# Kernel optimization log

Measured on AMD Instinct MI355X. Metric: run time of the kernel, lower is better.

Reference implementation:

```python
import jax, jax.numpy as jnp
import numpy as np

B, S, D, H = 2, 2048, 1024, 16
DK = D // H
NEG = -1e9


def setup_inputs() -> dict:
    key = jax.random.key(0)
    ks = jax.random.split(key, 12)
    inp = {
        "query": jax.random.normal(ks[0], (B, S, D), jnp.float32),
        "key": jax.random.normal(ks[1], (B, S, D), jnp.float32),
        "value": jax.random.normal(ks[2], (B, S, D), jnp.float32),
        "mask": jax.random.randint(ks[3], (B, S), 0, 2, jnp.int32),
    }
    # 4 linears (q, k, v, out), each d_model x d_model with bias.
    scale = 1.0 / np.sqrt(D)
    for i, name in enumerate(["wq", "wk", "wv", "wo"]):
        inp[name] = jax.random.uniform(ks[4 + i], (D, D), jnp.float32, -scale, scale)
        inp["b" + name[1]] = jax.random.uniform(ks[8 + i], (D,), jnp.float32, -scale, scale)
    return inp


def _split_heads(x):  # [B,S,D] -> [B,H,S,DK]
    return x.reshape(B, S, H, DK).transpose(0, 2, 1, 3)


def reference(query, key, value, mask, wq, bq, wk, bk, wv, bv, wo, bo):
    q = _split_heads(query @ wq.T + bq)
    k = _split_heads(key @ wk.T + bk)
    v = _split_heads(value @ wv.T + bv)
    scores = jnp.einsum("bhqd,bhkd->bhqk", q, k) / jnp.sqrt(jnp.float32(DK))
    # mask: [B,S] -> [B,1,1,S]; masked_fill where mask == 0
    m = mask[:, None, None, :]
    scores = jnp.where(m == 0, NEG, scores)
    attn = jax.nn.softmax(scores, axis=-1)  # dropout p=0 (eval) -> identity
    x = jnp.einsum("bhqk,bhkd->bhqd", attn, v)
    x = x.transpose(0, 2, 1, 3).reshape(B, S, D)
    return x @ wo.T + bo
```

## Files before the change

kernel.cpp:

```cpp
#include <hip/hip_runtime.h>


typedef _Float16 f16;
typedef _Float16 f16x8 __attribute__((ext_vector_type(8)));
typedef _Float16 f16x4 __attribute__((ext_vector_type(4)));
typedef __fp16 fp16x2r __attribute__((ext_vector_type(2)));
typedef float f32x4 __attribute__((ext_vector_type(4)));

#define MFMA_F16(a, b, c) __builtin_amdgcn_mfma_f32_16x16x32_f16((a), (b), (c), 0, 0, 0)
#define L2E 1.44269504088896340736f

__device__ __forceinline__ void gld16(const void* g, void* l) {
    __builtin_amdgcn_global_load_lds(
        (__attribute__((address_space(1))) void*)(g),
        (__attribute__((address_space(3))) void*)(l), 16, 0, 0);
}

__global__ __launch_bounds__(256) void cvt_kernel(
    const float* __restrict__ q, const float* __restrict__ k,
    const float* __restrict__ v,
    const float* __restrict__ wq, const float* __restrict__ wk,
    const float* __restrict__ wv, const float* __restrict__ wo,
    f16* __restrict__ oq, f16* __restrict__ ok, f16* __restrict__ ov,
    f16* __restrict__ owq, f16* __restrict__ owk, f16* __restrict__ owv,
    f16* __restrict__ owo)
{
    const int z = blockIdx.y;
    const float* src;
    f16* dst;
    int n;
    switch (z) {
        case 0: src = q;  dst = oq;  n = 4194304; break;
        case 1: src = k;  dst = ok;  n = 4194304; break;
        case 2: src = v;  dst = ov;  n = 4194304; break;
        case 3: src = wq; dst = owq; n = 1048576; break;
        case 4: src = wk; dst = owk; n = 1048576; break;
        case 5: src = wv; dst = owv; n = 1048576; break;
        default: src = wo; dst = owo; n = 1048576; break;
    }
    int idx = (blockIdx.x * 256 + threadIdx.x) * 8;
    if (idx >= n) return;
    float4 a = *(const float4*)(src + idx);
    float4 b = *(const float4*)(src + idx + 4);
    f16x8 h = { (f16)a.x, (f16)a.y, (f16)a.z, (f16)a.w,
                (f16)b.x, (f16)b.y, (f16)b.z, (f16)b.w };
    *(f16x8*)(dst + idx) = h;
}

__device__ __forceinline__ void stage_qkv(
    const f16* __restrict__ P0, const f16* __restrict__ P1,
    int blockM, int blockN, int k0, f16* Ad, f16* Bd,
    int wave, int srow2, int schunk)
{
#pragma unroll
    for (int p = 0; p < 2; p++) {
        int r0 = wave * 32 + p * 16;
        gld16(&P0[(size_t)(blockM + r0 + srow2) * 1024 + k0 + schunk * 8],
              &Ad[r0 * 32]);
        gld16(&P1[(size_t)(blockN + r0 + srow2) * 1024 + k0 + schunk * 8],
              &Bd[r0 * 32]);
    }
}

__global__ __launch_bounds__(256) void proj_qkv_kernel(
    const f16* __restrict__ xq, const f16* __restrict__ xk,
    const f16* __restrict__ xv,
    const f16* __restrict__ wqh, const f16* __restrict__ wkh,
    const f16* __restrict__ wvh,
    const float* __restrict__ bq, const float* __restrict__ bk,
    const float* __restrict__ bv,
    f16* __restrict__ qh, f16* __restrict__ kh, f16* __restrict__ vt)
{
    const int z = blockIdx.z;
    const f16* X = (z == 0) ? xq : (z == 1) ? xk : xv;
    const f16* W = (z == 0) ? wqh : (z == 1) ? wkh : wvh;
    const float* bias = (z == 0) ? bq : (z == 1) ? bk : bv;
    const f16* P0 = (z < 2) ? W : X;
    const f16* P1 = (z < 2) ? X : W;

    __shared__ __align__(16) f16 smem[24576];
    f16* L = smem;

    const int t = threadIdx.x;
    const int wave = t >> 6, lane = t & 63, quad = lane >> 4, l15 = lane & 15;
    const int m_base = (wave >> 1) * 64, n_base = (wave & 1) * 64;
    const int blockM = (z < 2) ? blockIdx.y * 128 : blockIdx.x * 128;
    const int blockN = (z < 2) ? blockIdx.x * 128 : blockIdx.y * 128;

    const int srow2 = lane >> 2;
    const int schunk = (lane & 3) ^ ((srow2 >> 1) & 3);
    const int rchunk = (l15 >> 1) & 3;

    f32x4 acc[4][4];
#pragma unroll
    for (int mt = 0; mt < 4; mt++)
#pragma unroll
        for (int nt = 0; nt < 4; nt++)
            acc[mt][nt] = (f32x4){0.f, 0.f, 0.f, 0.f};

    f16 *Ac = smem,          *An = smem + 4096,  *Af = smem + 8192;
    f16 *Bc = smem + 12288,  *Bn = smem + 16384, *Bf = smem + 20480;

    stage_qkv(P0, P1, blockM, blockN, 0,  Ac, Bc, wave, srow2, schunk);
    stage_qkv(P0, P1, blockM, blockN, 32, An, Bn, wave, srow2, schunk);
    asm volatile("s_waitcnt vmcnt(4)" ::: "memory");

    for (int ki = 0; ki < 32; ki++) {
        __builtin_amdgcn_s_barrier();
        __builtin_amdgcn_sched_barrier(0);
        if (ki < 30)
            stage_qkv(P0, P1, blockM, blockN, (ki + 2) * 32, Af, Bf,
                      wave, srow2, schunk);

        f16x8 af[4], bf[4];
#pragma unroll
        for (int mt = 0; mt < 4; mt++)
            af[mt] = *(const f16x8*)(&Ac[(m_base + mt * 16 + l15) * 32 +
                                         ((quad ^ rchunk) << 3)]);
#pragma unroll
        for (int nt = 0; nt < 4; nt++)
            bf[nt] = *(const f16x8*)(&Bc[(n_base + nt * 16 + l15) * 32 +
                                         ((quad ^ rchunk) << 3)]);
        __builtin_amdgcn_s_setprio(1);
#pragma unroll
        for (int mt = 0; mt < 4; mt++)
#pragma unroll
            for (int nt = 0; nt < 4; nt++)
                acc[mt][nt] = MFMA_F16(af[mt], bf[nt], acc[mt][nt]);
        __builtin_amdgcn_s_setprio(0);

        if (ki < 30)
            asm volatile("s_waitcnt vmcnt(4)" ::: "memory");
        else if (ki == 30)
            asm volatile("s_waitcnt vmcnt(0)" ::: "memory");
        f16* tA = Ac; Ac = An; An = Af; Af = tA;
        f16* tB = Bc; Bc = Bn; Bn = Bf; Bf = tB;
    }

    if (z < 2) {
        f16* o = (z == 0) ? qh : kh;
        const float scale = (z == 0) ? 0.125f * L2E : 1.0f;
        float4 b4[4];
#pragma unroll
        for (int mt = 0; mt < 4; mt++)
            b4[mt] = *(const float4*)(&bias[blockM + m_base + mt * 16 + quad * 4]);

#pragma unroll
        for (int half = 0; half < 2; half++) {
            __syncthreads();
            if ((wave & 1) == half) {
#pragma unroll
                for (int mt = 0; mt < 4; mt++)
#pragma unroll
                    for (int nt = 0; nt < 4; nt++) {
                        f16x4 pk = {
                            (f16)((acc[mt][nt][0] + b4[mt].x) * scale),
                            (f16)((acc[mt][nt][1] + b4[mt].y) * scale),
                            (f16)((acc[mt][nt][2] + b4[mt].z) * scale),
                            (f16)((acc[mt][nt][3] + b4[mt].w) * scale) };
                        *(f16x4*)(&L[(nt * 16 + l15) * 136 +
                                     m_base + mt * 16 + quad * 4]) = pk;
                    }
            }
            __syncthreads();
#pragma unroll
            for (int pass = 0; pass < 4; pass++) {
                int unit = pass * 32 + (t >> 3);
                int hh = unit >> 6, s_loc = unit & 63;
                f16x8 vv = *(const f16x8*)(&L[s_loc * 136 + hh * 64 + (t & 7) * 8]);
                int s_glob = blockN + half * 64 + s_loc;
                int b = s_glob >> 11, s = s_glob & 2047;
                int h_glob = (blockM >> 6) + hh;
                *(f16x8*)(&o[(((size_t)(b * 16 + h_glob) * 2048 + s) << 6) +
                             (t & 7) * 8]) = vv;
            }
        }
    } else {
        float bv_[4];
#pragma unroll
        for (int nt = 0; nt < 4; nt++)
            bv_[nt] = bias[blockN + n_base + nt * 16 + l15];

#pragma unroll
        for (int half = 0; half < 2; half++) {
            __syncthreads();
            if ((wave & 1) == half) {
#pragma unroll
                for (int mt = 0; mt < 4; mt++)
#pragma unroll
                    for (int nt = 0; nt < 4; nt++) {
                        f16x4 pk = { (f16)(acc[mt][nt][0] + bv_[nt]),
                                     (f16)(acc[mt][nt][1] + bv_[nt]),
                                     (f16)(acc[mt][nt][2] + bv_[nt]),
                                     (f16)(acc[mt][nt][3] + bv_[nt]) };
                        *(f16x4*)(&L[(nt * 16 + l15) * 136 +
                                     m_base + mt * 16 + quad * 4]) = pk;
                    }
            }
            __syncthreads();
#pragma unroll
            for (int pass = 0; pass < 4; pass++) {
                int f_loc = pass * 16 + (t >> 4);
                int tt = t & 15;
                int bb = (tt >= 8) ? 64 : 0;
                int o  = (tt & 7) * 8;
                int p  = (o >> 5) & 1;
                int c  = (o >> 3) & 3;
                int g1 = bb + p * 32 + c * 4;
                const f16* Lrow = &L[f_loc * 136];
                f16x4 lo = *(const f16x4*)(&Lrow[g1]);
                f16x4 hi = *(const f16x4*)(&Lrow[g1 + 16]);
                f16x8 vv = __builtin_shufflevector(lo, hi, 0, 1, 2, 3, 4, 5, 6, 7);
                int feat = blockN + half * 64 + f_loc;
                int hh = feat >> 6, dk = feat & 63;
                int b = blockM >> 11;
                int s0 = (blockM & 2047) + bb + o;
                *(f16x8*)(&vt[((size_t)((b * 16 + hh) * 64 + dk) << 11) + s0]) = vv;
            }
        }
    }
}

__device__ __forceinline__ void flash_stage2(
    const f16* kbase, const f16* vbase, int key0,
    f16* Kb, f16* Vb, int wg, int srow8, int sblk)
{
#pragma unroll
    for (int p = 0; p < 2; p++) {
        int r0 = wg * 16 + p * 8;
        int row = r0 + srow8;
        gld16(&kbase[(size_t)(key0 + row) * 64 + sblk * 8], &Kb[r0 * 64]);
        gld16(&vbase[(size_t)row * 2048 + key0 + sblk * 8], &Vb[r0 * 64]);
    }
}

__device__ __forceinline__ void flash_phase2(
    const f16* Kbuf, const f16* Vbuf, const float* bias_all, int key0,
    const f16x8 (&qf)[2][2], int quad, int l15,
    f32x4 (&O)[2][4], f32x4 (&lacc)[2])
{
    const int sw = l15 & 7;
    f32x4 sc[2][4];
#pragma unroll
    for (int nt = 0; nt < 4; nt++) {
        const f16* krow = &Kbuf[(nt * 16 + l15) * 64];
        f16x8 kf0 = *(const f16x8*)(&krow[(quad ^ sw) << 3]);
        f16x8 kf1 = *(const f16x8*)(&krow[((quad + 4) ^ sw) << 3]);
        float4 b4 = *(const float4*)(&bias_all[key0 + nt * 16 + quad * 4]);
        __builtin_amdgcn_s_setprio(1);
#pragma unroll
        for (int cb = 0; cb < 2; cb++) {
            f32x4 z4 = (f32x4){b4.x, b4.y, b4.z, b4.w};
            z4 = MFMA_F16(kf0, qf[cb][0], z4);
            sc[cb][nt] = MFMA_F16(kf1, qf[cb][1], z4);
        }
        __builtin_amdgcn_s_setprio(0);
    }
    const f16x8 ones8 = {(f16)1.f, (f16)1.f, (f16)1.f, (f16)1.f,
                         (f16)1.f, (f16)1.f, (f16)1.f, (f16)1.f};
    union P8u { f16x8 v8; fp16x2r h[4]; };
    P8u pp[2][2];
#pragma unroll
    for (int cb = 0; cb < 2; cb++) {
#pragma unroll
        for (int nt = 0; nt < 4; nt++) {
            float p0 = __builtin_amdgcn_exp2f(sc[cb][nt][0]);
            float p1 = __builtin_amdgcn_exp2f(sc[cb][nt][1]);
            float p2 = __builtin_amdgcn_exp2f(sc[cb][nt][2]);
            float p3 = __builtin_amdgcn_exp2f(sc[cb][nt][3]);
            pp[cb][nt >> 1].h[(nt & 1) * 2 + 0] = __builtin_amdgcn_cvt_pkrtz(p0, p1);
            pp[cb][nt >> 1].h[(nt & 1) * 2 + 1] = __builtin_amdgcn_cvt_pkrtz(p2, p3);
        }
        lacc[cb] = MFMA_F16(ones8, pp[cb][0].v8, lacc[cb]);
        lacc[cb] = MFMA_F16(ones8, pp[cb][1].v8, lacc[cb]);
    }
    __builtin_amdgcn_s_setprio(1);
#pragma unroll
    for (int nto = 0; nto < 4; nto++) {
        const f16* vrow = &Vbuf[(nto * 16 + l15) * 64];
        f16x8 va = *(const f16x8*)(&vrow[(quad ^ sw) << 3]);
        f16x8 vb = *(const f16x8*)(&vrow[((4 + quad) ^ sw) << 3]);
#pragma unroll
        for (int cb = 0; cb < 2; cb++) {
            O[cb][nto] = MFMA_F16(va, pp[cb][0].v8, O[cb][nto]);
            O[cb][nto] = MFMA_F16(vb, pp[cb][1].v8, O[cb][nto]);
        }
    }
    __builtin_amdgcn_s_setprio(0);
}

__global__
__attribute__((amdgpu_flat_work_group_size(512, 512)))
__attribute__((amdgpu_waves_per_eu(4, 4)))
void flash_kernel(
    const f16* __restrict__ qh, const f16* __restrict__ kh,
    const f16* __restrict__ vt, const int* __restrict__ mask,
    f16* __restrict__ ctx)
{
    __shared__ __align__(16) f16 KV[8 * 4096];
    __shared__ float bias_all[2048];

    const int t = threadIdx.x;
    const int wave = t >> 6, lane = t & 63, quad = lane >> 4, l15 = lane & 15;
    const int group = wave >> 2, wg = wave & 3;
    const int bh = blockIdx.x;
    const int b = bh >> 4, h = bh & 15;
    const int q0 = blockIdx.y * 128;

    const f16* qbase = qh + (size_t)bh * (2048 * 64);
    const f16* kbase = kh + (size_t)bh * (2048 * 64);
    const f16* vbase = vt + (size_t)bh * (64 * 2048);

    f16* K0 = &KV[((0 * 2 + group) * 2 + 0) * 4096];
    f16* V0 = &KV[((0 * 2 + group) * 2 + 1) * 4096];
    f16* K1 = &KV[((1 * 2 + group) * 2 + 0) * 4096];
    f16* V1 = &KV[((1 * 2 + group) * 2 + 1) * 4096];

#pragma unroll
    for (int j = 0; j < 4; j++) {
        int i = j * 512 + t;
        bias_all[i] = (mask[b * 2048 + i] == 0) ? -1.0e9f : 0.0f;
    }

    f16x8 qf[2][2];
#pragma unroll
    for (int cb = 0; cb < 2; cb++) {
        int qrow = q0 + wg * 32 + cb * 16 + l15;
        qf[cb][0] = *(const f16x8*)(&qbase[qrow * 64 + quad * 8]);
        qf[cb][1] = *(const f16x8*)(&qbase[qrow * 64 + 32 + quad * 8]);
    }

    f32x4 O[2][4];
#pragma unroll
    for (int cb = 0; cb < 2; cb++)
#pragma unroll
        for (int n = 0; n < 4; n++) O[cb][n] = (f32x4){0.f, 0.f, 0.f, 0.f};
    f32x4 lacc[2] = {(f32x4){0.f, 0.f, 0.f, 0.f}, (f32x4){0.f, 0.f, 0.f, 0.f}};

    const int srow8 = lane >> 3;
    const int sblk = (lane & 7) ^ srow8;

    flash_stage2(kbase, vbase, group * 64, K0, V0, wg, srow8, sblk);

    for (int k2 = 0; k2 < 16; k2 += 2) {
        __syncthreads();
        flash_stage2(kbase, vbase, (k2 + 1) * 128 + group * 64, K1, V1,
                     wg, srow8, sblk);
        flash_phase2(K0, V0, bias_all, k2 * 128 + group * 64,
                     qf, quad, l15, O, lacc);
        __syncthreads();
        if (k2 < 14)
            flash_stage2(kbase, vbase, (k2 + 2) * 128 + group * 64, K0, V0,
                         wg, srow8, sblk);
        flash_phase2(K1, V1, bias_all, (k2 + 1) * 128 + group * 64,
                     qf, quad, l15, O, lacc);
    }

    __syncthreads();
    float* Red = (float*)KV;
    const int t4 = wg * 64 + lane;
    if (group == 1) {
#pragma unroll
        for (int cb = 0; cb < 2; cb++) {
#pragma unroll
            for (int nto = 0; nto < 4; nto++)
                *(f32x4*)(&Red[(cb * 4 + nto) * 1024 + t4 * 4]) = O[cb][nto];
            Red[8 * 1024 + cb * 256 + t4] = lacc[cb][0];
        }
    }
    __syncthreads();
    if (group == 0) {
#pragma unroll
        for (int cb = 0; cb < 2; cb++) {
            const float l2 = Red[8 * 1024 + cb * 256 + t4];
            const float inv_l = 1.0f / (lacc[cb][0] + l2);
            int qrow = q0 + wg * 32 + cb * 16 + l15;
#pragma unroll
            for (int nto = 0; nto < 4; nto++) {
                f32x4 o2 = *(const f32x4*)(&Red[(cb * 4 + nto) * 1024 + t4 * 4]);
                f16x4 pk = { (f16)((O[cb][nto][0] + o2[0]) * inv_l),
                             (f16)((O[cb][nto][1] + o2[1]) * inv_l),
                             (f16)((O[cb][nto][2] + o2[2]) * inv_l),
                             (f16)((O[cb][nto][3] + o2[3]) * inv_l) };
                *(f16x4*)(&ctx[(size_t)(b * 2048 + qrow) * 1024 + h * 64 +
                               nto * 16 + quad * 4]) = pk;
            }
        }
    }
}

__device__ __forceinline__ void stage_out(
    const f16* __restrict__ ctx, const f16* __restrict__ woh,
    int blockM, int blockN, int k0, f16* Ad, f16* Bd,
    int wave, int srow2, int schunk)
{
#pragma unroll
    for (int p = 0; p < 2; p++) {
        int r0 = wave * 32 + p * 16;
        gld16(&ctx[(size_t)(blockM + r0 + srow2) * 1024 + k0 + schunk * 8],
              &Ad[r0 * 32]);
    }
    {
        int r0 = wave * 16;
        gld16(&woh[(size_t)(blockN + r0 + srow2) * 1024 + k0 + schunk * 8],
              &Bd[r0 * 32]);
    }
}

__global__ __launch_bounds__(256) void proj_out_kernel(
    const f16* __restrict__ ctx, const f16* __restrict__ woh,
    const float* __restrict__ bo, float* __restrict__ out)
{
    __shared__ __align__(16) f16 smem[18432];

    const int t = threadIdx.x;
    const int wave = t >> 6, lane = t & 63, quad = lane >> 4, l15 = lane & 15;
    const int m_base = (wave >> 1) * 64, n_base = (wave & 1) * 32;
    const int blockM = blockIdx.x * 128;
    const int blockN = blockIdx.y * 64;

    const int srow2 = lane >> 2;
    const int schunk = (lane & 3) ^ ((srow2 >> 1) & 3);
    const int rchunk = (l15 >> 1) & 3;

    f32x4 acc[4][2];
#pragma unroll
    for (int mt = 0; mt < 4; mt++)
#pragma unroll
        for (int nt = 0; nt < 2; nt++)
            acc[mt][nt] = (f32x4){0.f, 0.f, 0.f, 0.f};

    f16 *Ac = smem,          *An = smem + 4096,  *Af = smem + 8192;
    f16 *Bc = smem + 12288,  *Bn = smem + 14336, *Bf = smem + 16384;

    stage_out(ctx, woh, blockM, blockN, 0,  Ac, Bc, wave, srow2, schunk);
    stage_out(ctx, woh, blockM, blockN, 32, An, Bn, wave, srow2, schunk);
    asm volatile("s_waitcnt vmcnt(3)" ::: "memory");

    for (int ki = 0; ki < 32; ki++) {
        __builtin_amdgcn_s_barrier();
        __builtin_amdgcn_sched_barrier(0);
        if (ki < 30)
            stage_out(ctx, woh, blockM, blockN, (ki + 2) * 32, Af, Bf,
                      wave, srow2, schunk);

        f16x8 af[4], bf[2];
#pragma unroll
        for (int mt = 0; mt < 4; mt++)
            af[mt] = *(const f16x8*)(&Ac[(m_base + mt * 16 + l15) * 32 +
                                         ((quad ^ rchunk) << 3)]);
#pragma unroll
        for (int nt = 0; nt < 2; nt++)
            bf[nt] = *(const f16x8*)(&Bc[(n_base + nt * 16 + l15) * 32 +
                                         ((quad ^ rchunk) << 3)]);
        __builtin_amdgcn_s_setprio(1);
#pragma unroll
        for (int mt = 0; mt < 4; mt++)
#pragma unroll
            for (int nt = 0; nt < 2; nt++)
                acc[mt][nt] = MFMA_F16(af[mt], bf[nt], acc[mt][nt]);
        __builtin_amdgcn_s_setprio(0);

        if (ki < 30)
            asm volatile("s_waitcnt vmcnt(3)" ::: "memory");
        else if (ki == 30)
            asm volatile("s_waitcnt vmcnt(0)" ::: "memory");
        f16* tA = Ac; Ac = An; An = Af; Af = tA;
        f16* tB = Bc; Bc = Bn; Bn = Bf; Bf = tB;
    }

    float bo_[2];
#pragma unroll
    for (int nt = 0; nt < 2; nt++)
        bo_[nt] = bo[blockN + n_base + nt * 16 + l15];

#pragma unroll
    for (int mt = 0; mt < 4; mt++) {
        int row0 = blockM + m_base + mt * 16 + quad * 4;
#pragma unroll
        for (int nt = 0; nt < 2; nt++) {
            int col_g = blockN + n_base + nt * 16 + l15;
#pragma unroll
            for (int i = 0; i < 4; i++)
                out[(size_t)(row0 + i) * 1024 + col_g] = acc[mt][nt][i] + bo_[nt];
        }
    }
}

extern "C" void kernel_launch(void* const* d_in, const int* in_sizes, int n_in,
                              void* d_out, int out_size, void* d_ws, size_t ws_size,
                              hipStream_t stream) {
    const float* query = (const float*)d_in[0];
    const float* key_  = (const float*)d_in[1];
    const float* value = (const float*)d_in[2];
    const int*   mask  = (const int*)d_in[3];
    const float* wq = (const float*)d_in[4];
    const float* bq = (const float*)d_in[5];
    const float* wk = (const float*)d_in[6];
    const float* bk = (const float*)d_in[7];
    const float* wv = (const float*)d_in[8];
    const float* bv = (const float*)d_in[9];
    const float* wo = (const float*)d_in[10];
    const float* bo = (const float*)d_in[11];
    float* out = (float*)d_out;

    f16* xq  = (f16*)d_ws;
    f16* xk  = xq  + 4194304;
    f16* xv  = xk  + 4194304;
    f16* wqh = xv  + 4194304;
    f16* wkh = wqh + 1048576;
    f16* wvh = wkh + 1048576;
    f16* woh = wvh + 1048576;
    f16* qh  = woh + 1048576;
    f16* kh  = qh  + 4194304;
    f16* vt  = kh  + 4194304;
    f16* ctx = xq;

    cvt_kernel<<<dim3(2048, 7), 256, 0, stream>>>(
        query, key_, value, wq, wk, wv, wo, xq, xk, xv, wqh, wkh, wvh, woh);
    proj_qkv_kernel<<<dim3(32, 8, 3), 256, 0, stream>>>(
        xq, xk, xv, wqh, wkh, wvh, bq, bk, bv, qh, kh, vt);
    flash_kernel<<<dim3(32, 16), 512, 0, stream>>>(qh, kh, vt, mask, ctx);
    proj_out_kernel<<<dim3(32, 16), 256, 0, stream>>>(ctx, woh, bo, out);
}
```

Measured before the change: 209.6 us.

## Restructure flash loop into K double-buffer with single V buffer and fp16 bias

Splits the K/V staging so K is double-buffered while V uses a single buffer that is loaded during the QK^T/softmax phase and consumed after a barrier. Shared memory shrinks from 8 to 6 tiles, and the mask bias becomes fp16, which cuts LDS use further. The waves-per-EU hint is raised so more workgroups can be resident. In exchange there are now two barriers per 128-key step instead of one per step pair, and V loads have less time to land before they are used.

```diff
diff --git a/kernel.cpp b/kernel.cpp
--- a/kernel.cpp
+++ b/kernel.cpp
@@ -9,6 +9,8 @@
 
 #define MFMA_F16(a, b, c) __builtin_amdgcn_mfma_f32_16x16x32_f16((a), (b), (c), 0, 0, 0)
 #define L2E 1.44269504088896340736f
+
+union P8u { f16x8 v8; fp16x2r h[4]; };
 
 __device__ __forceinline__ void gld16(const void* g, void* l) {
     __builtin_amdgcn_global_load_lds(
@@ -221,23 +223,30 @@
     }
 }
 
-__device__ __forceinline__ void flash_stage2(
-    const f16* kbase, const f16* vbase, int key0,
-    f16* Kb, f16* Vb, int wg, int srow8, int sblk)
+__device__ __forceinline__ void stageK2(
+    const f16* kbase, int key0, f16* Kb, int wg, int srow8, int sblk)
 {
 #pragma unroll
     for (int p = 0; p < 2; p++) {
         int r0 = wg * 16 + p * 8;
-        int row = r0 + srow8;
-        gld16(&kbase[(size_t)(key0 + row) * 64 + sblk * 8], &Kb[r0 * 64]);
-        gld16(&vbase[(size_t)row * 2048 + key0 + sblk * 8], &Vb[r0 * 64]);
-    }
-}
-
-__device__ __forceinline__ void flash_phase2(
-    const f16* Kbuf, const f16* Vbuf, const float* bias_all, int key0,
+        gld16(&kbase[(size_t)(key0 + r0 + srow8) * 64 + sblk * 8], &Kb[r0 * 64]);
+    }
+}
+
+__device__ __forceinline__ void stageV2(
+    const f16* vbase, int key0, f16* Vb, int wg, int srow8, int sblk)
+{
+#pragma unroll
+    for (int p = 0; p < 2; p++) {
+        int r0 = wg * 16 + p * 8;
+        gld16(&vbase[(size_t)(r0 + srow8) * 2048 + key0 + sblk * 8], &Vb[r0 * 64]);
+    }
+}
+
+__device__ __forceinline__ void flash_qk2(
+    const f16* Kbuf, const f16* bias16, int key0,
     const f16x8 (&qf)[2][2], int quad, int l15,
-    f32x4 (&O)[2][4], f32x4 (&lacc)[2])
+    P8u (&pp)[2][2], f32x4 (&lacc)[2])
 {
     const int sw = l15 & 7;
     f32x4 sc[2][4];
@@ -246,11 +255,12 @@
         const f16* krow = &Kbuf[(nt * 16 + l15) * 64];
         f16x8 kf0 = *(const f16x8*)(&krow[(quad ^ sw) << 3]);
         f16x8 kf1 = *(const f16x8*)(&krow[((quad + 4) ^ sw) << 3]);
-        float4 b4 = *(const float4*)(&bias_all[key0 + nt * 16 + quad * 4]);
+        f16x4 bh = *(const f16x4*)(&bias16[key0 + nt * 16 + quad * 4]);
+        f32x4 zb = {(float)bh[0], (float)bh[1], (float)bh[2], (float)bh[3]};
         __builtin_amdgcn_s_setprio(1);
 #pragma unroll
         for (int cb = 0; cb < 2; cb++) {
-            f32x4 z4 = (f32x4){b4.x, b4.y, b4.z, b4.w};
+            f32x4 z4 = zb;
             z4 = MFMA_F16(kf0, qf[cb][0], z4);
             sc[cb][nt] = MFMA_F16(kf1, qf[cb][1], z4);
         }
@@ -258,8 +268,6 @@
     }
     const f16x8 ones8 = {(f16)1.f, (f16)1.f, (f16)1.f, (f16)1.f,
                          (f16)1.f, (f16)1.f, (f16)1.f, (f16)1.f};
-    union P8u { f16x8 v8; fp16x2r h[4]; };
-    P8u pp[2][2];
 #pragma unroll
     for (int cb = 0; cb < 2; cb++) {
 #pragma unroll
@@ -274,6 +282,13 @@
         lacc[cb] = MFMA_F16(ones8, pp[cb][0].v8, lacc[cb]);
         lacc[cb] = MFMA_F16(ones8, pp[cb][1].v8, lacc[cb]);
     }
+}
+
+__device__ __forceinline__ void flash_pv2(
+    const f16* Vbuf, const P8u (&pp)[2][2], int quad, int l15,
+    f32x4 (&O)[2][4])
+{
+    const int sw = l15 & 7;
     __builtin_amdgcn_s_setprio(1);
 #pragma unroll
     for (int nto = 0; nto < 4; nto++) {
@@ -291,14 +306,14 @@
 
 __global__
 __attribute__((amdgpu_flat_work_group_size(512, 512)))
-__attribute__((amdgpu_waves_per_eu(4, 4)))
+__attribute__((amdgpu_waves_per_eu(6, 8)))
 void flash_kernel(
     const f16* __restrict__ qh, const f16* __restrict__ kh,
     const f16* __restrict__ vt, const int* __restrict__ mask,
     f16* __restrict__ ctx)
 {
-    __shared__ __align__(16) f16 KV[8 * 4096];
-    __shared__ float bias_all[2048];
+    __shared__ __align__(16) f16 KV[6 * 4096];
+    __shared__ __align__(16) f16 bias16[2048];
 
     const int t = threadIdx.x;
     const int wave = t >> 6, lane = t & 63, quad = lane >> 4, l15 = lane & 15;
@@ -311,15 +326,14 @@
     const f16* kbase = kh + (size_t)bh * (2048 * 64);
     const f16* vbase = vt + (size_t)bh * (64 * 2048);
 
-    f16* K0 = &KV[((0 * 2 + group) * 2 + 0) * 4096];
-    f16* V0 = &KV[((0 * 2 + group) * 2 + 1) * 4096];
-    f16* K1 = &KV[((1 * 2 + group) * 2 + 0) * 4096];
-    f16* V1 = &KV[((1 * 2 + group) * 2 + 1) * 4096];
+    f16* Ka  = &KV[(group * 3 + 0) * 4096];
+    f16* Kb_ = &KV[(group * 3 + 1) * 4096];
+    f16* Vb  = &KV[(group * 3 + 2) * 4096];
 
 #pragma unroll
     for (int j = 0; j < 4; j++) {
         int i = j * 512 + t;
-        bias_all[i] = (mask[b * 2048 + i] == 0) ? -1.0e9f : 0.0f;
+        bias16[i] = (mask[b * 2048 + i] == 0) ? (f16)(-65504.f) : (f16)0.f;
     }
 
     f16x8 qf[2][2];
@@ -340,23 +354,23 @@
     const int srow8 = lane >> 3;
     const int sblk = (lane & 7) ^ srow8;
 
-    flash_stage2(kbase, vbase, group * 64, K0, V0, wg, srow8, sblk);
-
-    for (int k2 = 0; k2 < 16; k2 += 2) {
+    stageK2(kbase, group * 64, Ka, wg, srow8, sblk);
+    __syncthreads();
+
+    f16 *Kc = Ka, *Kn = Kb_;
+    for (int s = 0; s < 16; s++) {
+        const int key0 = s * 128 + group * 64;
+        stageV2(vbase, key0, Vb, wg, srow8, sblk);
+        if (s < 15)
+            stageK2(kbase, key0 + 128, Kn, wg, srow8, sblk);
+        P8u pp[2][2];
+        flash_qk2(Kc, bias16, key0, qf, quad, l15, pp, lacc);
         __syncthreads();
-        flash_stage2(kbase, vbase, (k2 + 1) * 128 + group * 64, K1, V1,
-                     wg, srow8, sblk);
-        flash_phase2(K0, V0, bias_all, k2 * 128 + group * 64,
-                     qf, quad, l15, O, lacc);
+        flash_pv2(Vb, pp, quad, l15, O);
         __syncthreads();
-        if (k2 < 14)
-            flash_stage2(kbase, vbase, (k2 + 2) * 128 + group * 64, K0, V0,
-                         wg, srow8, sblk);
-        flash_phase2(K1, V1, bias_all, (k2 + 1) * 128 + group * 64,
-                     qf, quad, l15, O, lacc);
-    }
-
-    __syncthreads();
+        f16* tk = Kc; Kc = Kn; Kn = tk;
+    }
+
     float* Red = (float*)KV;
     const int t4 = wg * 64 + lane;
     if (group == 1) {
```

Result: slower. 444.4 us (+112.1%).
